# Kernel optimization log

Measured on AMD Instinct MI355X. Metric: run time of the kernel, lower is better.

The kernel has to match this reference:

```python
import jax, jax.numpy as jnp
import numpy as np

N_EMBD = 768
N_EXPERTS = 8
TOP_K = 2
D_FF = 4 * N_EMBD


def setup_inputs() -> dict:
    key = jax.random.key(0)
    k1, k2, k3, k4 = jax.random.split(key, 4)
    x = jax.random.normal(k1, (2, 2048, N_EMBD), dtype=jnp.float32)
    gate_w = jax.random.normal(k2, (N_EMBD, N_EXPERTS), dtype=jnp.float32) * (1.0 / np.sqrt(N_EMBD))
    w_fc = jax.random.normal(k3, (N_EXPERTS, N_EMBD, D_FF), dtype=jnp.float32) * (1.0 / np.sqrt(N_EMBD))
    w_proj = jax.random.normal(k4, (N_EXPERTS, D_FF, N_EMBD), dtype=jnp.float32) * (1.0 / np.sqrt(D_FF))
    return {"x": x, "gate_w": gate_w, "w_fc": w_fc, "w_proj": w_proj}


def reference(x, gate_w, w_fc, w_proj):
    B, S, D = x.shape
    E = w_fc.shape[0]
    xt = x.reshape(-1, D)                    # [T, D]
    T = xt.shape[0]
    scores = xt @ gate_w                      # [T, E]
    expert_weights, expert_indices = jax.lax.top_k(scores, TOP_K)  # [T, K]
    expert_weights = jax.nn.softmax(expert_weights, axis=-1)
    # per-token combine weight for each expert (0 if expert not selected)
    comb = jnp.zeros((T, E), dtype=xt.dtype)
    comb = comb.at[jnp.arange(T)[:, None], expert_indices].add(expert_weights)  # [T, E]
    out = jnp.zeros_like(xt)
    for e in range(E):  # fixed small loop over experts
        h = jax.nn.gelu(xt @ w_fc[e], approximate=False)  # torch nn.GELU default = exact erf
        y_e = h @ w_proj[e]                               # [T, D]
        out = out + comb[:, e:e + 1] * y_e
    return out.reshape(B, S, D)
```

## Files before the change

kernel.cpp:

```cpp
#include <hip/hip_runtime.h>
#include <hip/hip_bf16.h>
#include <math.h>

#define T_TOK 4096
#define D_EMB 768
#define DFF   3072
#define N_EXP 8
#define MAXT  72
#define CNTS  16

typedef __attribute__((ext_vector_type(8))) short bf16x8;
typedef __attribute__((ext_vector_type(4))) float f32x4;

__device__ __forceinline__ short f2bf(float f) {
  union { __hip_bfloat16 b; short s; } u;
  u.b = __float2bfloat16(f);
  return u.s;
}

__device__ __forceinline__ float gelu_f(float v) {
  float u = 0.7978845608f * v * (1.0f + 0.044715f * v * v);
  float a = fabsf(u);
  float em = __expf(-2.0f * a);
  float th = (1.0f - em) / (1.0f + em);
  th = (u < 0.0f) ? -th : th;
  return 0.5f * v * (1.0f + th);
}

__device__ __forceinline__ int swz(int row) { return (row ^ (row >> 2)) & 3; }

__global__ void zero_init_kernel(float4* __restrict__ out4, int n4, int* __restrict__ cnt) {
  int i = blockIdx.x * blockDim.x + threadIdx.x;
  if (i < N_EXP * CNTS) cnt[i] = 0;
  float4 z; z.x = z.y = z.z = z.w = 0.f;
  for (int j = i; j < n4; j += gridDim.x * blockDim.x) out4[j] = z;
}

__global__ __launch_bounds__(256)
void slab_weights(const float* __restrict__ src, short* __restrict__ dst,
                  int Kt, int Nt, int NCT, int NKTall) {
  __shared__ float t32[32][132];
  int ct = blockIdx.x, kt = blockIdx.y, e = blockIdx.z;
  const float* s = src + ((size_t)e * Kt + kt * 32) * Nt + ct * 128;
  int tid = threadIdx.x;
#pragma unroll
  for (int p4 = 0; p4 < 4; p4++) {
    int idx = tid + p4 * 256;
    int kl = idx >> 5, c4 = idx & 31;
    float4 v = *(const float4*)&s[(size_t)kl * Nt + c4 * 4];
    t32[kl][c4 * 4 + 0] = v.x; t32[kl][c4 * 4 + 1] = v.y;
    t32[kl][c4 * 4 + 2] = v.z; t32[kl][c4 * 4 + 3] = v.w;
  }
  __syncthreads();
  short* d = dst + (((size_t)e * NCT + ct) * NKTall + kt) * 4096;
#pragma unroll
  for (int i = 0; i < 2; i++) {
    int seg = tid + i * 256;
    int row = seg >> 2, p = seg & 3;
    int q = p ^ swz(row);
    union { short sv[8]; uint4 u; } o;
#pragma unroll
    for (int j = 0; j < 8; j++) o.sv[j] = f2bf(t32[q * 8 + j][row]);
    *(uint4*)&d[(size_t)seg * 8] = o.u;
  }
}

__global__ __launch_bounds__(256)
void gate_kernel(const float* __restrict__ x, const float* __restrict__ gw,
                 int* __restrict__ cnt, int* __restrict__ tok,
                 float* __restrict__ wgt) {
  __shared__ int lcnt[N_EXP];
  __shared__ int gbase[N_EXP];
  __shared__ int le[32];
  __shared__ float lw[32];
  __shared__ int lpos[32];
  int tid = threadIdx.x, lane = tid & 63, wid = tid >> 6;
  if (tid < N_EXP) lcnt[tid] = 0;
  __syncthreads();

#pragma unroll
  for (int i = 0; i < 4; i++) {
    int t = blockIdx.x * 16 + wid * 4 + i;
    float s[N_EXP];
#pragma unroll
    for (int e = 0; e < N_EXP; e++) s[e] = 0.f;
#pragma unroll
    for (int dd = 0; dd < D_EMB / 64; dd++) {
      int d = dd * 64 + lane;
      float xv = x[(size_t)t * D_EMB + d];
#pragma unroll
      for (int e = 0; e < N_EXP; e++) s[e] += xv * gw[d * N_EXP + e];
    }
#pragma unroll
    for (int e = 0; e < N_EXP; e++) {
#pragma unroll
      for (int off = 32; off > 0; off >>= 1) s[e] += __shfl_xor(s[e], off, 64);
    }
    if (lane == 0) {
      int e0 = 0;
#pragma unroll
      for (int e = 1; e < N_EXP; e++) if (s[e] > s[e0]) e0 = e;
      int e1 = -1;
#pragma unroll
      for (int e = 0; e < N_EXP; e++) {
        if (e == e0) continue;
        if (e1 < 0 || s[e] > s[e1]) e1 = e;
      }
      float p1 = __expf(s[e1] - s[e0]);
      float inv = 1.f / (1.f + p1);
      int idx = (wid * 4 + i) * 2;
      le[idx] = e0; lw[idx] = inv;           lpos[idx] = atomicAdd(&lcnt[e0], 1);
      le[idx + 1] = e1; lw[idx + 1] = p1 * inv; lpos[idx + 1] = atomicAdd(&lcnt[e1], 1);
    }
  }
  __syncthreads();
  if (tid < N_EXP) gbase[tid] = atomicAdd(&cnt[tid * CNTS], lcnt[tid]);
  __syncthreads();
  if (tid < 32) {
    int e = le[tid];
    int t = blockIdx.x * 16 + (tid >> 1);
    int p = gbase[e] + lpos[tid];
    tok[e * T_TOK + p] = t;
    wgt[e * T_TOK + p] = lw[tid];
  }
}

__global__ void plan_kernel(const int* __restrict__ cnt, int* __restrict__ offs,
                            int* __restrict__ tile_e, int* __restrict__ tile_rt,
                            int* __restrict__ ntiles) {
  if (threadIdx.x != 0 || blockIdx.x != 0) return;
  int o = 0, nt = 0;
  for (int e = 0; e < N_EXP; e++) {
    offs[e] = o;
    int tc = (cnt[e * CNTS] + 127) >> 7;
    for (int i = 0; i < tc; i++) { tile_e[nt] = e; tile_rt[nt] = i; nt++; }
    o += cnt[e * CNTS];
  }
  *ntiles = nt;
}

__global__ __launch_bounds__(256)
void gatherA_kernel(const float* __restrict__ x, const int* __restrict__ tok,
                    const int* __restrict__ cnt, const int* __restrict__ offs,
                    const int* __restrict__ tile_e, const int* __restrict__ tile_rt,
                    const int* __restrict__ ntiles, short* __restrict__ aslab) {
  int tile = blockIdx.x, kt = blockIdx.y;
  if (tile >= *ntiles) return;
  int e = tile_e[tile], rt = tile_rt[tile];
  int ne = cnt[e * CNTS];
  int tid = threadIdx.x;
  short* d = aslab + ((size_t)tile * 24 + kt) * 4096;
#pragma unroll
  for (int i = 0; i < 2; i++) {
    int seg = tid + i * 256;
    int row = seg >> 2, p = seg & 3;
    int q = p ^ swz(row);
    int r = rt * 128 + row; if (r >= ne) r = ne - 1;
    int t = tok[e * T_TOK + r];
    const float* src = x + (size_t)t * D_EMB + kt * 32 + q * 8;
    union { short sv[8]; uint4 u; } o;
#pragma unroll
    for (int j = 0; j < 8; j++) o.sv[j] = f2bf(src[j]);
    *(uint4*)&d[(size_t)seg * 8] = o.u;
  }
}

template<int KDIM, int NDIM, int SPLITK, int GRT, int GCT, int EPI>
__global__ __launch_bounds__(256, 2)
void pipe_gemm(const short* __restrict__ Aop, const short* __restrict__ Bslab,
               const int* __restrict__ tok, const float* __restrict__ wgt,
               const int* __restrict__ cnt, const int* __restrict__ offs,
               const int* __restrict__ tile_e, const int* __restrict__ tile_rt,
               const int* __restrict__ ntiles,
               short* __restrict__ hout, float* __restrict__ fout) {
  const int COLT = NDIM / 128;
  const int KS = KDIM / SPLITK;
  const int NKT = KS / 32;
  const int NKTALL = KDIM / 32;
  const int ASTRIDE = (EPI == 0) ? 4096 : 32;
  const int BPS = GRT * GCT;
  const int NCG = COLT / GCT;
  const int PER_SK = MAXT * COLT;
  static_assert(NKT % 4 == 0 && NKT >= 8, "depth-4 pipeline needs NKT%4==0");

  int nwg = gridDim.x, cpx = nwg >> 3;
  int logical = (blockIdx.x & 7) * cpx + (blockIdx.x >> 3);
  int sk = logical / PER_SK;
  int rem = logical % PER_SK;
  int super = rem / BPS, inner = rem % BPS;
  int band = super / NCG, cg = super % NCG;
  int tile = band * GRT + (inner % GRT);
  int ct = cg * GCT + (inner / GRT);
  if (tile >= *ntiles) return;
  int e = tile_e[tile], rt = tile_rt[tile];
  int ne = cnt[e * CNTS];
  int base = offs[e];

  __shared__ __align__(16) short As[2][4096];
  __shared__ __align__(16) short Bs[2][4096];

  int tid = threadIdx.x, lane = tid & 63, wid = tid >> 6;
  int wr = (wid >> 1) * 64, wc = (wid & 1) * 64;
  int cb = lane >> 4;

  const short* ap0;
  const short* ap1;
  if (EPI == 0) {
    ap0 = Aop + (size_t)tile * NKTALL * 4096 + tid * 8;
    ap1 = ap0 + 2048;
  } else {
    {
      int seg = tid;
      int row = seg >> 2, p = seg & 3;
      int q = p ^ swz(row);
      int r = rt * 128 + row; if (r >= ne) r = ne - 1;
      ap0 = Aop + (size_t)(base + r) * KDIM + sk * KS + q * 8;
    }
    {
      int seg = tid + 256;
      int row = seg >> 2, p = seg & 3;
      int q = p ^ swz(row);
      int r = rt * 128 + row; if (r >= ne) r = ne - 1;
      ap1 = Aop + (size_t)(base + r) * KDIM + sk * KS + q * 8;
    }
  }
  const short* bp0 = Bslab + (((size_t)e * COLT + ct) * NKTALL + sk * NKT) * 4096 + tid * 8;
  const short* bp1 = bp0 + 2048;
  int lo0 = tid * 8, lo1 = (tid + 256) * 8;

  int offa[4], offb[4];
#pragma unroll
  for (int m = 0; m < 4; m++) {
    int row = wr + m * 16 + (lane & 15);
    offa[m] = row * 32 + ((cb ^ swz(row)) * 8);
  }
#pragma unroll
  for (int n = 0; n < 4; n++) {
    int row = wc + n * 16 + (lane & 15);
    offb[n] = row * 32 + ((cb ^ swz(row)) * 8);
  }

  f32x4 acc[4][4];
#pragma unroll
  for (int m = 0; m < 4; m++)
#pragma unroll
    for (int n = 0; n < 4; n++) acc[m][n] = (f32x4){0.f, 0.f, 0.f, 0.f};

  f32x4 rA0a, rA0b, rB0a, rB0b;
  f32x4 rA1a, rA1b, rB1a, rB1b;
  f32x4 rA2a, rA2b, rB2a, rB2b;
  f32x4 rA3a, rA3b, rB3a, rB3b;

#define LOADS(LA0, LA1, LB0, LB1, KT) do {                                    \
    LA0 = *(const f32x4*)(ap0 + (size_t)(KT) * ASTRIDE);                      \
    LA1 = *(const f32x4*)(ap1 + (size_t)(KT) * ASTRIDE);                      \
    LB0 = *(const f32x4*)(bp0 + (size_t)(KT) * 4096);                        \
    LB1 = *(const f32x4*)(bp1 + (size_t)(KT) * 4096);                        \
  } while (0)
#define WRITES(WA0, WA1, WB0, WB1, LW) do {                                   \
    *(f32x4*)&As[LW][lo0] = WA0; *(f32x4*)&As[LW][lo1] = WA1;                 \
    *(f32x4*)&Bs[LW][lo0] = WB0; *(f32x4*)&Bs[LW][lo1] = WB1;                 \
  } while (0)
#define COMPUTE(LR) do {                                                      \
    bf16x8 af_[4], bv_[4];                                                    \
    _Pragma("unroll") for (int m_ = 0; m_ < 4; ++m_)                          \
      af_[m_] = *(const bf16x8*)&As[LR][offa[m_]];                            \
    _Pragma("unroll") for (int n_ = 0; n_ < 4; ++n_)                          \
      bv_[n_] = *(const bf16x8*)&Bs[LR][offb[n_]];                            \
    _Pragma("unroll") for (int m_ = 0; m_ < 4; ++m_)                          \
      _Pragma("unroll") for (int n_ = 0; n_ < 4; ++n_)                        \
        acc[m_][n_] = __builtin_amdgcn_mfma_f32_16x16x32_bf16(                \
            af_[m_], bv_[n_], acc[m_][n_], 0, 0, 0);                          \
  } while (0)
#define ENDSTEP() do {                                                        \
    asm volatile("s_waitcnt lgkmcnt(0)" ::: "memory");                        \
    __builtin_amdgcn_sched_barrier(0);                                        \
    __builtin_amdgcn_s_barrier();                                             \
  } while (0)
#define STEP(LR, LW, WA0, WA1, WB0, WB1, LA0, LA1, LB0, LB1, KT, DOLD, DOWR) do { \
    if (DOLD) LOADS(LA0, LA1, LB0, LB1, (KT));                                \
    if (DOWR) WRITES(WA0, WA1, WB0, WB1, (LW));                               \
    COMPUTE(LR);                                                              \
    ENDSTEP();                                                                \
  } while (0)

  LOADS(rA0a, rA0b, rB0a, rB0b, 0);
  LOADS(rA1a, rA1b, rB1a, rB1b, 1);
  LOADS(rA2a, rA2b, rB2a, rB2b, 2);
  LOADS(rA3a, rA3b, rB3a, rB3b, 3);
  WRITES(rA0a, rA0b, rB0a, rB0b, 0);
  ENDSTEP();

#pragma unroll 1
  for (int g = 0; g < (NKT - 4) / 4; ++g) {
    int kb = 4 * g;
    STEP(0, 1, rA1a, rA1b, rB1a, rB1b, rA0a, rA0b, rB0a, rB0b, kb + 4, 1, 1);
    STEP(1, 0, rA2a, rA2b, rB2a, rB2b, rA1a, rA1b, rB1a, rB1b, kb + 5, 1, 1);
    STEP(0, 1, rA3a, rA3b, rB3a, rB3b, rA2a, rA2b, rB2a, rB2b, kb + 6, 1, 1);
    STEP(1, 0, rA0a, rA0b, rB0a, rB0b, rA3a, rA3b, rB3a, rB3b, kb + 7, 1, 1);
  }
  STEP(0, 1, rA1a, rA1b, rB1a, rB1b, rA0a, rA0b, rB0a, rB0b, 0, 0, 1);
  STEP(1, 0, rA2a, rA2b, rB2a, rB2b, rA1a, rA1b, rB1a, rB1b, 0, 0, 1);
  STEP(0, 1, rA3a, rA3b, rB3a, rB3b, rA2a, rA2b, rB2a, rB2b, 0, 0, 1);
  STEP(1, 0, rA0a, rA0b, rB0a, rB0b, rA3a, rA3b, rB3a, rB3b, 0, 0, 0);

#undef STEP
#undef ENDSTEP
#undef COMPUTE
#undef WRITES
#undef LOADS

  int colbase = ct * 128 + wc;
#pragma unroll
  for (int m = 0; m < 4; m++) {
#pragma unroll
    for (int j = 0; j < 4; j++) {
      int rloc = rt * 128 + wr + m * 16 + ((lane >> 4) << 2) + j;
      if (rloc < ne) {
        if (EPI == 0) {
          size_t hrow = (size_t)(base + rloc) * NDIM;
#pragma unroll
          for (int n = 0; n < 4; n++)
            hout[hrow + colbase + n * 16 + (lane & 15)] = f2bf(gelu_f(acc[m][n][j]));
        } else {
          int t = tok[e * T_TOK + rloc];
          float w = wgt[e * T_TOK + rloc];
          float* orow = fout + (size_t)t * NDIM + colbase + (lane & 15);
#pragma unroll
          for (int n = 0; n < 4; n++)
            atomicAdd(orow + n * 16, w * acc[m][n][j]);
        }
      }
    }
  }
}

extern "C" void kernel_launch(void* const* d_in, const int* in_sizes, int n_in,
                              void* d_out, int out_size, void* d_ws, size_t ws_size,
                              hipStream_t stream) {
  const float* x   = (const float*)d_in[0];
  const float* gw  = (const float*)d_in[1];
  const float* wfc = (const float*)d_in[2];
  const float* wpj = (const float*)d_in[3];
  float* out = (float*)d_out;

  char* ws = (char*)d_ws;
  const size_t SZ_ASLAB = (size_t)MAXT * 24 * 4096 * 2;
  const size_t SZ_BFC   = (size_t)N_EXP * 24 * 24 * 4096 * 2;
  const size_t SZ_BPJ   = (size_t)N_EXP * 6 * 96 * 4096 * 2;
  const size_t SZ_H     = (size_t)2 * T_TOK * DFF * 2;
  short* aslab = (short*)(ws);
  short* bfc   = (short*)(ws + SZ_ASLAB);
  short* bpj   = (short*)(ws + SZ_ASLAB + SZ_BFC);
  short* h     = (short*)(ws + SZ_ASLAB + SZ_BFC + SZ_BPJ);
  char* p2     = ws + SZ_ASLAB + SZ_BFC + SZ_BPJ + SZ_H;
  int*   tok  = (int*)(p2);
  float* wgt  = (float*)(p2 + (size_t)N_EXP * T_TOK * 4);
  char* p3    = p2 + (size_t)N_EXP * T_TOK * 8;
  int*   cnt     = (int*)(p3);
  int*   offs    = (int*)(p3 + 1024);
  int*   tile_e  = (int*)(p3 + 1024 + 64);
  int*   tile_rt = (int*)(p3 + 1024 + 64 + 512);
  int*   ntiles  = (int*)(p3 + 1024 + 64 + 1024);

  int n4 = out_size / 4;
  zero_init_kernel<<<2048, 256, 0, stream>>>((float4*)out, n4, cnt);
  slab_weights<<<dim3(24, 24, N_EXP), 256, 0, stream>>>(wfc, bfc, D_EMB, DFF, 24, 24);
  slab_weights<<<dim3(6, 96, N_EXP), 256, 0, stream>>>(wpj, bpj, DFF, D_EMB, 6, 96);
  gate_kernel<<<T_TOK / 16, 256, 0, stream>>>(x, gw, cnt, tok, wgt);
  plan_kernel<<<1, 1, 0, stream>>>(cnt, offs, tile_e, tile_rt, ntiles);
  gatherA_kernel<<<dim3(MAXT, 24), 256, 0, stream>>>(x, tok, cnt, offs, tile_e, tile_rt, ntiles, aslab);
  pipe_gemm<D_EMB, DFF, 1, 8, 8, 0><<<MAXT * (DFF / 128), 256, 0, stream>>>(
      aslab, bfc, tok, wgt, cnt, offs, tile_e, tile_rt, ntiles, h, nullptr);
  pipe_gemm<DFF, D_EMB, 4, 8, 6, 1><<<4 * MAXT * (D_EMB / 128), 256, 0, stream>>>(
      h, bpj, tok, wgt, cnt, offs, tile_e, tile_rt, ntiles, nullptr, out);
}
```

Before: 250.0 us.

## Double K-step per barrier in grouped GEMM and halve split-K for projection

The MFMA main loop now handles two 32-wide K slices per barrier. It uses 64-wide shared-memory stages and a depth-2 register prefetch instead of a depth-4 pipeline over 32-wide slices. This halves the number of barriers and waitcnt stalls per K and gives the MFMA units larger bursts of work between syncs. The down-projection GEMM also drops from split-K 4 to 2, which halves the atomic accumulation traffic into the output and the number of workgroups. In exchange, LDS use doubles to 64KB per block, which may limit occupancy, and prefetch depth in K-steps is shallower.

```diff
diff --git a/kernel.cpp b/kernel.cpp
--- a/kernel.cpp
+++ b/kernel.cpp
@@ -175,13 +175,15 @@
                short* __restrict__ hout, float* __restrict__ fout) {
   const int COLT = NDIM / 128;
   const int KS = KDIM / SPLITK;
-  const int NKT = KS / 32;
+  const int NK32 = KS / 32;
+  const int NST = NK32 / 2;
   const int NKTALL = KDIM / 32;
-  const int ASTRIDE = (EPI == 0) ? 4096 : 32;
+  const int ASTEP = (EPI == 0) ? 8192 : 64;
+  const int ASUB  = (EPI == 0) ? 4096 : 32;
   const int BPS = GRT * GCT;
   const int NCG = COLT / GCT;
   const int PER_SK = MAXT * COLT;
-  static_assert(NKT % 4 == 0 && NKT >= 8, "depth-4 pipeline needs NKT%4==0");
+  static_assert(NST % 2 == 0 && NST >= 4, "fat-step pipe needs NST%2==0");
 
   int nwg = gridDim.x, cpx = nwg >> 3;
   int logical = (blockIdx.x & 7) * cpx + (blockIdx.x >> 3);
@@ -196,8 +198,8 @@
   int ne = cnt[e * CNTS];
   int base = offs[e];
 
-  __shared__ __align__(16) short As[2][4096];
-  __shared__ __align__(16) short Bs[2][4096];
+  __shared__ __align__(16) short As[2][8192];
+  __shared__ __align__(16) short Bs[2][8192];
 
   int tid = threadIdx.x, lane = tid & 63, wid = tid >> 6;
   int wr = (wid >> 1) * 64, wc = (wid & 1) * 64;
@@ -224,7 +226,7 @@
       ap1 = Aop + (size_t)(base + r) * KDIM + sk * KS + q * 8;
     }
   }
-  const short* bp0 = Bslab + (((size_t)e * COLT + ct) * NKTALL + sk * NKT) * 4096 + tid * 8;
+  const short* bp0 = Bslab + (((size_t)e * COLT + ct) * NKTALL + sk * NK32) * 4096 + tid * 8;
   const short* bp1 = bp0 + 2048;
   int lo0 = tid * 8, lo1 = (tid + 256) * 8;
 
@@ -246,65 +248,66 @@
 #pragma unroll
     for (int n = 0; n < 4; n++) acc[m][n] = (f32x4){0.f, 0.f, 0.f, 0.f};
 
-  f32x4 rA0a, rA0b, rB0a, rB0b;
-  f32x4 rA1a, rA1b, rB1a, rB1b;
-  f32x4 rA2a, rA2b, rB2a, rB2b;
-  f32x4 rA3a, rA3b, rB3a, rB3b;
-
-#define LOADS(LA0, LA1, LB0, LB1, KT) do {                                    \
-    LA0 = *(const f32x4*)(ap0 + (size_t)(KT) * ASTRIDE);                      \
-    LA1 = *(const f32x4*)(ap1 + (size_t)(KT) * ASTRIDE);                      \
-    LB0 = *(const f32x4*)(bp0 + (size_t)(KT) * 4096);                        \
-    LB1 = *(const f32x4*)(bp1 + (size_t)(KT) * 4096);                        \
+  f32x4 s0a0, s0a1, s0a2, s0a3, s0b0, s0b1, s0b2, s0b3;
+  f32x4 s1a0, s1a1, s1a2, s1a3, s1b0, s1b1, s1b2, s1b3;
+
+#define LOADS(A0, A1, A2, A3, B0, B1, B2, B3, T) do {                         \
+    A0 = *(const f32x4*)(ap0 + (size_t)(T) * ASTEP);                          \
+    A1 = *(const f32x4*)(ap1 + (size_t)(T) * ASTEP);                          \
+    A2 = *(const f32x4*)(ap0 + (size_t)(T) * ASTEP + ASUB);                   \
+    A3 = *(const f32x4*)(ap1 + (size_t)(T) * ASTEP + ASUB);                   \
+    B0 = *(const f32x4*)(bp0 + (size_t)(T) * 8192);                          \
+    B1 = *(const f32x4*)(bp1 + (size_t)(T) * 8192);                          \
+    B2 = *(const f32x4*)(bp0 + (size_t)(T) * 8192 + 4096);                   \
+    B3 = *(const f32x4*)(bp1 + (size_t)(T) * 8192 + 4096);                   \
   } while (0)
-#define WRITES(WA0, WA1, WB0, WB1, LW) do {                                   \
-    *(f32x4*)&As[LW][lo0] = WA0; *(f32x4*)&As[LW][lo1] = WA1;                 \
-    *(f32x4*)&Bs[LW][lo0] = WB0; *(f32x4*)&Bs[LW][lo1] = WB1;                 \
+#define WRITES(A0, A1, A2, A3, B0, B1, B2, B3, L) do {                        \
+    *(f32x4*)&As[L][lo0] = A0;        *(f32x4*)&As[L][lo1] = A1;              \
+    *(f32x4*)&As[L][lo0 + 4096] = A2; *(f32x4*)&As[L][lo1 + 4096] = A3;       \
+    *(f32x4*)&Bs[L][lo0] = B0;        *(f32x4*)&Bs[L][lo1] = B1;              \
+    *(f32x4*)&Bs[L][lo0 + 4096] = B2; *(f32x4*)&Bs[L][lo1 + 4096] = B3;       \
   } while (0)
-#define COMPUTE(LR) do {                                                      \
-    bf16x8 af_[4], bv_[4];                                                    \
-    _Pragma("unroll") for (int m_ = 0; m_ < 4; ++m_)                          \
-      af_[m_] = *(const bf16x8*)&As[LR][offa[m_]];                            \
-    _Pragma("unroll") for (int n_ = 0; n_ < 4; ++n_)                          \
-      bv_[n_] = *(const bf16x8*)&Bs[LR][offb[n_]];                            \
-    _Pragma("unroll") for (int m_ = 0; m_ < 4; ++m_)                          \
+#define COMPUTE(L) do {                                                       \
+    _Pragma("unroll") for (int s_ = 0; s_ < 2; ++s_) {                        \
+      bf16x8 af_[4], bv_[4];                                                  \
+      _Pragma("unroll") for (int m_ = 0; m_ < 4; ++m_)                        \
+        af_[m_] = *(const bf16x8*)&As[L][s_ * 4096 + offa[m_]];               \
       _Pragma("unroll") for (int n_ = 0; n_ < 4; ++n_)                        \
-        acc[m_][n_] = __builtin_amdgcn_mfma_f32_16x16x32_bf16(                \
-            af_[m_], bv_[n_], acc[m_][n_], 0, 0, 0);                          \
+        bv_[n_] = *(const bf16x8*)&Bs[L][s_ * 4096 + offb[n_]];               \
+      _Pragma("unroll") for (int m_ = 0; m_ < 4; ++m_)                        \
+        _Pragma("unroll") for (int n_ = 0; n_ < 4; ++n_)                      \
+          acc[m_][n_] = __builtin_amdgcn_mfma_f32_16x16x32_bf16(              \
+              af_[m_], bv_[n_], acc[m_][n_], 0, 0, 0);                        \
+    }                                                                         \
   } while (0)
 #define ENDSTEP() do {                                                        \
     asm volatile("s_waitcnt lgkmcnt(0)" ::: "memory");                        \
     __builtin_amdgcn_sched_barrier(0);                                        \
     __builtin_amdgcn_s_barrier();                                             \
   } while (0)
-#define STEP(LR, LW, WA0, WA1, WB0, WB1, LA0, LA1, LB0, LB1, KT, DOLD, DOWR) do { \
-    if (DOLD) LOADS(LA0, LA1, LB0, LB1, (KT));                                \
-    if (DOWR) WRITES(WA0, WA1, WB0, WB1, (LW));                               \
-    COMPUTE(LR);                                                              \
-    ENDSTEP();                                                                \
-  } while (0)
-
-  LOADS(rA0a, rA0b, rB0a, rB0b, 0);
-  LOADS(rA1a, rA1b, rB1a, rB1b, 1);
-  LOADS(rA2a, rA2b, rB2a, rB2b, 2);
-  LOADS(rA3a, rA3b, rB3a, rB3b, 3);
-  WRITES(rA0a, rA0b, rB0a, rB0b, 0);
+
+  LOADS(s0a0, s0a1, s0a2, s0a3, s0b0, s0b1, s0b2, s0b3, 0);
+  LOADS(s1a0, s1a1, s1a2, s1a3, s1b0, s1b1, s1b2, s1b3, 1);
+  WRITES(s0a0, s0a1, s0a2, s0a3, s0b0, s0b1, s0b2, s0b3, 0);
   ENDSTEP();
 
 #pragma unroll 1
-  for (int g = 0; g < (NKT - 4) / 4; ++g) {
-    int kb = 4 * g;
-    STEP(0, 1, rA1a, rA1b, rB1a, rB1b, rA0a, rA0b, rB0a, rB0b, kb + 4, 1, 1);
-    STEP(1, 0, rA2a, rA2b, rB2a, rB2b, rA1a, rA1b, rB1a, rB1b, kb + 5, 1, 1);
-    STEP(0, 1, rA3a, rA3b, rB3a, rB3b, rA2a, rA2b, rB2a, rB2b, kb + 6, 1, 1);
-    STEP(1, 0, rA0a, rA0b, rB0a, rB0b, rA3a, rA3b, rB3a, rB3b, kb + 7, 1, 1);
-  }
-  STEP(0, 1, rA1a, rA1b, rB1a, rB1b, rA0a, rA0b, rB0a, rB0b, 0, 0, 1);
-  STEP(1, 0, rA2a, rA2b, rB2a, rB2b, rA1a, rA1b, rB1a, rB1b, 0, 0, 1);
-  STEP(0, 1, rA3a, rA3b, rB3a, rB3b, rA2a, rA2b, rB2a, rB2b, 0, 0, 1);
-  STEP(1, 0, rA0a, rA0b, rB0a, rB0b, rA3a, rA3b, rB3a, rB3b, 0, 0, 0);
-
-#undef STEP
+  for (int g = 0; g < (NST - 2) / 2; ++g) {
+    int t = 2 * g;
+    WRITES(s1a0, s1a1, s1a2, s1a3, s1b0, s1b1, s1b2, s1b3, 1);
+    LOADS(s0a0, s0a1, s0a2, s0a3, s0b0, s0b1, s0b2, s0b3, t + 2);
+    COMPUTE(0);
+    ENDSTEP();
+    WRITES(s0a0, s0a1, s0a2, s0a3, s0b0, s0b1, s0b2, s0b3, 0);
+    LOADS(s1a0, s1a1, s1a2, s1a3, s1b0, s1b1, s1b2, s1b3, t + 3);
+    COMPUTE(1);
+    ENDSTEP();
+  }
+  WRITES(s1a0, s1a1, s1a2, s1a3, s1b0, s1b1, s1b2, s1b3, 1);
+  COMPUTE(0);
+  ENDSTEP();
+  COMPUTE(1);
+
 #undef ENDSTEP
 #undef COMPUTE
 #undef WRITES
@@ -372,6 +375,6 @@
   gatherA_kernel<<<dim3(MAXT, 24), 256, 0, stream>>>(x, tok, cnt, offs, tile_e, tile_rt, ntiles, aslab);
   pipe_gemm<D_EMB, DFF, 1, 8, 8, 0><<<MAXT * (DFF / 128), 256, 0, stream>>>(
       aslab, bfc, tok, wgt, cnt, offs, tile_e, tile_rt, ntiles, h, nullptr);
-  pipe_gemm<DFF, D_EMB, 4, 8, 6, 1><<<4 * MAXT * (D_EMB / 128), 256, 0, stream>>>(
+  pipe_gemm<DFF, D_EMB, 2, 8, 6, 1><<<2 * MAXT * (D_EMB / 128), 256, 0, stream>>>(
       h, bpj, tok, wgt, cnt, offs, tile_e, tile_rt, ntiles, nullptr, out);
 }
```

Result: faster. 224.2 us (-10.3%).

## Switch GEMM pipeline to triple-buffered LDS with relaxed waits and halve split-K

Applied to the files above, without the earlier changes.

Replaces the double-buffered LDS plus four-deep register prefetch with three LDS buffers and three register stages. Each step now computes from one buffer, writes the next, and issues global loads, waiting only to lgkmcnt(4) so the latest LDS writes can stay in flight across the barrier. This frees registers and raises the launch-bounds occupancy target to 3 blocks per CU. The aim is better latency hiding and more resident waves, at the cost of 48KB of LDS per block. The down-projection GEMM also drops split-K from 4 to 2, which halves the atomic partial-sum traffic but also halves that GEMM's grid.

```diff
diff --git a/kernel.cpp b/kernel.cpp
--- a/kernel.cpp
+++ b/kernel.cpp
@@ -166,7 +166,7 @@
 }
 
 template<int KDIM, int NDIM, int SPLITK, int GRT, int GCT, int EPI>
-__global__ __launch_bounds__(256, 2)
+__global__ __launch_bounds__(256, 3)
 void pipe_gemm(const short* __restrict__ Aop, const short* __restrict__ Bslab,
                const int* __restrict__ tok, const float* __restrict__ wgt,
                const int* __restrict__ cnt, const int* __restrict__ offs,
@@ -181,7 +181,7 @@
   const int BPS = GRT * GCT;
   const int NCG = COLT / GCT;
   const int PER_SK = MAXT * COLT;
-  static_assert(NKT % 4 == 0 && NKT >= 8, "depth-4 pipeline needs NKT%4==0");
+  static_assert(NKT % 3 == 0 && NKT >= 9, "3-buffer pipeline needs NKT%3==0");
 
   int nwg = gridDim.x, cpx = nwg >> 3;
   int logical = (blockIdx.x & 7) * cpx + (blockIdx.x >> 3);
@@ -196,8 +196,8 @@
   int ne = cnt[e * CNTS];
   int base = offs[e];
 
-  __shared__ __align__(16) short As[2][4096];
-  __shared__ __align__(16) short Bs[2][4096];
+  __shared__ __align__(16) short As[3][4096];
+  __shared__ __align__(16) short Bs[3][4096];
 
   int tid = threadIdx.x, lane = tid & 63, wid = tid >> 6;
   int wr = (wid >> 1) * 64, wc = (wid & 1) * 64;
@@ -249,7 +249,6 @@
   f32x4 rA0a, rA0b, rB0a, rB0b;
   f32x4 rA1a, rA1b, rB1a, rB1b;
   f32x4 rA2a, rA2b, rB2a, rB2b;
-  f32x4 rA3a, rA3b, rB3a, rB3b;
 
 #define LOADS(LA0, LA1, LB0, LB1, KT) do {                                    \
     LA0 = *(const f32x4*)(ap0 + (size_t)(KT) * ASTRIDE);                      \
@@ -272,40 +271,40 @@
         acc[m_][n_] = __builtin_amdgcn_mfma_f32_16x16x32_bf16(                \
             af_[m_], bv_[n_], acc[m_][n_], 0, 0, 0);                          \
   } while (0)
-#define ENDSTEP() do {                                                        \
+#define END4() do {                                                           \
+    asm volatile("s_waitcnt lgkmcnt(4)" ::: "memory");                        \
+    __builtin_amdgcn_sched_barrier(0);                                        \
+    __builtin_amdgcn_s_barrier();                                             \
+  } while (0)
+#define END0() do {                                                           \
     asm volatile("s_waitcnt lgkmcnt(0)" ::: "memory");                        \
     __builtin_amdgcn_sched_barrier(0);                                        \
     __builtin_amdgcn_s_barrier();                                             \
   } while (0)
-#define STEP(LR, LW, WA0, WA1, WB0, WB1, LA0, LA1, LB0, LB1, KT, DOLD, DOWR) do { \
-    if (DOLD) LOADS(LA0, LA1, LB0, LB1, (KT));                                \
-    if (DOWR) WRITES(WA0, WA1, WB0, WB1, (LW));                               \
-    COMPUTE(LR);                                                              \
-    ENDSTEP();                                                                \
-  } while (0)
 
   LOADS(rA0a, rA0b, rB0a, rB0b, 0);
   LOADS(rA1a, rA1b, rB1a, rB1b, 1);
   LOADS(rA2a, rA2b, rB2a, rB2b, 2);
-  LOADS(rA3a, rA3b, rB3a, rB3b, 3);
   WRITES(rA0a, rA0b, rB0a, rB0b, 0);
-  ENDSTEP();
+  WRITES(rA1a, rA1b, rB1a, rB1b, 1);
+  END0();
 
 #pragma unroll 1
-  for (int g = 0; g < (NKT - 4) / 4; ++g) {
-    int kb = 4 * g;
-    STEP(0, 1, rA1a, rA1b, rB1a, rB1b, rA0a, rA0b, rB0a, rB0b, kb + 4, 1, 1);
-    STEP(1, 0, rA2a, rA2b, rB2a, rB2b, rA1a, rA1b, rB1a, rB1b, kb + 5, 1, 1);
-    STEP(0, 1, rA3a, rA3b, rB3a, rB3b, rA2a, rA2b, rB2a, rB2b, kb + 6, 1, 1);
-    STEP(1, 0, rA0a, rA0b, rB0a, rB0b, rA3a, rA3b, rB3a, rB3b, kb + 7, 1, 1);
-  }
-  STEP(0, 1, rA1a, rA1b, rB1a, rB1b, rA0a, rA0b, rB0a, rB0b, 0, 0, 1);
-  STEP(1, 0, rA2a, rA2b, rB2a, rB2b, rA1a, rA1b, rB1a, rB1b, 0, 0, 1);
-  STEP(0, 1, rA3a, rA3b, rB3a, rB3b, rA2a, rA2b, rB2a, rB2b, 0, 0, 1);
-  STEP(1, 0, rA0a, rA0b, rB0a, rB0b, rA3a, rA3b, rB3a, rB3b, 0, 0, 0);
-
-#undef STEP
-#undef ENDSTEP
+  for (int g = 0; g < (NKT - 6) / 3; ++g) {
+    int kb = 3 * g;
+    COMPUTE(0); WRITES(rA2a, rA2b, rB2a, rB2b, 2); LOADS(rA0a, rA0b, rB0a, rB0b, kb + 3); END4();
+    COMPUTE(1); WRITES(rA0a, rA0b, rB0a, rB0b, 0); LOADS(rA1a, rA1b, rB1a, rB1b, kb + 4); END4();
+    COMPUTE(2); WRITES(rA1a, rA1b, rB1a, rB1b, 1); LOADS(rA2a, rA2b, rB2a, rB2b, kb + 5); END4();
+  }
+  COMPUTE(0); WRITES(rA2a, rA2b, rB2a, rB2b, 2); LOADS(rA0a, rA0b, rB0a, rB0b, NKT - 3); END4();
+  COMPUTE(1); WRITES(rA0a, rA0b, rB0a, rB0b, 0); LOADS(rA1a, rA1b, rB1a, rB1b, NKT - 2); END4();
+  COMPUTE(2); WRITES(rA1a, rA1b, rB1a, rB1b, 1); LOADS(rA2a, rA2b, rB2a, rB2b, NKT - 1); END4();
+  COMPUTE(0); WRITES(rA2a, rA2b, rB2a, rB2b, 2); END4();
+  COMPUTE(1); END0();
+  COMPUTE(2);
+
+#undef END0
+#undef END4
 #undef COMPUTE
 #undef WRITES
 #undef LOADS
@@ -372,6 +371,6 @@
   gatherA_kernel<<<dim3(MAXT, 24), 256, 0, stream>>>(x, tok, cnt, offs, tile_e, tile_rt, ntiles, aslab);
   pipe_gemm<D_EMB, DFF, 1, 8, 8, 0><<<MAXT * (DFF / 128), 256, 0, stream>>>(
       aslab, bfc, tok, wgt, cnt, offs, tile_e, tile_rt, ntiles, h, nullptr);
-  pipe_gemm<DFF, D_EMB, 4, 8, 6, 1><<<4 * MAXT * (D_EMB / 128), 256, 0, stream>>>(
+  pipe_gemm<DFF, D_EMB, 2, 8, 6, 1><<<2 * MAXT * (D_EMB / 128), 256, 0, stream>>>(
       h, bpj, tok, wgt, cnt, offs, tile_e, tile_rt, ntiles, nullptr, out);
 }
```

Result: faster. 213.3 us (-14.6%).
